# Kernel tuning notes

Measured on AMD Instinct MI355X. Metric: run time of the kernel, lower is better.

## Reference

```python
import jax, jax.numpy as jnp
import numpy as np

DIM = 512
T = 65536


def setup_inputs() -> dict:
    key = jax.random.key(0)
    k1, = jax.random.split(key, 1)
    z_rest = jax.random.normal(k1, (T, DIM), dtype=jnp.float32)
    # var_vbl = inv_softplus(sqrt(var_init)) with var_init=1.0 -> log(expm1(1.0))
    var_vbl = jnp.full((DIM,), float(np.log(np.expm1(1.0))), dtype=jnp.float32)
    # corr_vbl = inv_sigmoid(0.1) = log(0.1) - log(0.9)
    corr_vbl = jnp.full((DIM,), float(np.log(0.1) - np.log(0.9)), dtype=jnp.float32)
    prior_mu = jnp.zeros((DIM,), dtype=jnp.float32)
    return {"z_rest": z_rest, "var_vbl": var_vbl, "corr_vbl": corr_vbl, "prior_mu": prior_mu}


def reference(z_rest, var_vbl, corr_vbl, prior_mu):
    # init_train_lkd with z_context=None, starting from fresh state (sample_size=0).
    prior_var = jnp.square(jax.nn.softplus(var_vbl))          # [D]
    prior_cov = jax.nn.sigmoid(corr_vbl) * prior_var          # [D]
    two_pi = 2.0 * jnp.pi

    def step(carry, xs):
        mu, var, lkd = carry
        z, t = xs  # z: [D], t: scalar step index (== sample_size - 1 after increment)
        lkd = lkd + jnp.sum(-0.5 * jnp.log(two_pi * var)
                            - jnp.square(z - mu) / (2.0 * var))
        dd = prior_cov / (prior_var + prior_cov * t)
        mu = (1.0 - dd) * mu + z * dd
        var = (1.0 - dd) * var + (prior_var - prior_cov) * dd
        return (mu, var, lkd), None

    ts = jnp.arange(z_rest.shape[0], dtype=z_rest.dtype)
    init = (prior_mu.astype(z_rest.dtype), prior_var, jnp.zeros((), z_rest.dtype))
    (_, _, lkd), _ = jax.lax.scan(step, init, (z_rest, ts))
    return lkd
```

## Files before the change

### kernel.cpp

```cpp
#include <hip/hip_runtime.h>
#include <math.h>


#define DIM    512
#define TT     65536
#define CHUNKS 1024
#define ROWS   64
#define GROUPS 64
#define CPG    16

#define TWO_PI 6.283185307179586

__global__ __launch_bounds__(128) void k1_fused(const float* __restrict__ z,
                                                const float* __restrict__ var_vbl,
                                                const float* __restrict__ corr_vbl,
                                                const float* __restrict__ prior_mu,
                                                float* __restrict__ sums,
                                                float* __restrict__ s0a,
                                                float* __restrict__ s1a,
                                                float* __restrict__ s2a) {
    const int chunk = blockIdx.x;
    const int tid = threadIdx.x;
    const int d0 = tid * 4;
    const float t0m1 = (float)(chunk * ROWS) - 1.0f;

    float vv[4], cc[4], k0[4], L[4], S0[4], S1[4], S2[4], Dprev[4], invDprev[4];
#pragma unroll
    for (int j = 0; j < 4; ++j) {
        const int d = d0 + j;
        float spv = log1pf(expf(var_vbl[d]));
        float v = spv * spv;
        float c = v / (1.0f + expf(-corr_vbl[d]));
        vv[j] = v;
        cc[j] = c;
        k0[j] = (v - c) * prior_mu[d];
        L[j] = 0.f; S0[j] = 0.f; S1[j] = 0.f; S2[j] = 0.f;
        Dprev[j] = fmaf(c, t0m1, v);
        invDprev[j] = __builtin_amdgcn_rcpf(Dprev[j]);
    }

    const float4* zp = reinterpret_cast<const float4*>(z)
                       + (size_t)chunk * ROWS * (DIM / 4) + tid;
    float tf = t0m1 + 1.0f;
#pragma unroll 4
    for (int r = 0; r < ROWS; ++r) {
        float4 zv = zp[(size_t)r * (DIM / 4)];
        float zz[4] = {zv.x, zv.y, zv.z, zv.w};
#pragma unroll
        for (int j = 0; j < 4; ++j) {
            float Dt = fmaf(cc[j], tf, vv[j]);
            float invDt = __builtin_amdgcn_rcpf(Dt);
            float w = fmaf(Dprev[j], zz[j], -fmaf(cc[j], L[j], k0[j]));
            float rr = invDt * invDprev[j];
            S0[j] += rr;
            float rw = rr * w;
            S1[j] += rw;
            S2[j] = fmaf(rw, w, S2[j]);
            L[j] += zz[j];
            Dprev[j] = Dt;
            invDprev[j] = invDt;
        }
        tf += 1.0f;
    }

    const size_t o4 = (size_t)chunk * (DIM / 4) + tid;
    reinterpret_cast<float4*>(sums)[o4] = make_float4(L[0], L[1], L[2], L[3]);
    reinterpret_cast<float4*>(s0a)[o4] = make_float4(S0[0], S0[1], S0[2], S0[3]);
    reinterpret_cast<float4*>(s1a)[o4] = make_float4(S1[0], S1[1], S1[2], S1[3]);
    reinterpret_cast<float4*>(s2a)[o4] = make_float4(S2[0], S2[1], S2[2], S2[3]);
}

__global__ __launch_bounds__(512) void k2a_gsum(const float* __restrict__ sums,
                                                float* __restrict__ gsums) {
    const int g = blockIdx.x;
    const int d = threadIdx.x;
    float vals[CPG];
#pragma unroll
    for (int i = 0; i < CPG; ++i)
        vals[i] = sums[(size_t)(g * CPG + i) * DIM + d];
    float run = 0.f;
#pragma unroll
    for (int i = 0; i < CPG; ++i) run += vals[i];
    gsums[(size_t)g * DIM + d] = run;
}

__global__ __launch_bounds__(512) void k2b_scan(float* __restrict__ gsums,
                                                const float* __restrict__ var_vbl,
                                                const float* __restrict__ corr_vbl,
                                                float* __restrict__ out) {
    const int d = threadIdx.x;
    float vals[GROUPS];
#pragma unroll
    for (int g = 0; g < GROUPS; ++g)
        vals[g] = gsums[(size_t)g * DIM + d];
    float run = 0.f;
#pragma unroll
    for (int g = 0; g < GROUPS; ++g) {
        gsums[(size_t)g * DIM + d] = run;
        run += vals[g];
    }
    double sp = log1p(exp((double)var_vbl[d]));
    double v = sp * sp;
    double cc = v / (1.0 + exp(-(double)corr_vbl[d]));
    double vmc = v - cc;
    double Dlast = v + cc * (double)(TT - 1);
    double Ld = -0.5 * ((double)TT * (log(TWO_PI) + log(vmc)) + log(Dlast / vmc));
    __shared__ double red[512];
    red[d] = Ld;
    __syncthreads();
    for (int s = 256; s > 0; s >>= 1) {
        if (d < s) red[d] += red[d + s];
        __syncthreads();
    }
    if (d == 0) out[0] = (float)red[0];
}

__global__ __launch_bounds__(512) void k2c_combine(const float* __restrict__ sums,
                                                   const float* __restrict__ gsums,
                                                   const float* __restrict__ s0a,
                                                   const float* __restrict__ s1a,
                                                   const float* __restrict__ s2a,
                                                   const float* __restrict__ var_vbl,
                                                   const float* __restrict__ corr_vbl,
                                                   float* __restrict__ out) {
    const int g = blockIdx.x;
    const int d = threadIdx.x;
    float spv = log1pf(expf(var_vbl[d]));
    float v = spv * spv;
    float c = v / (1.0f + expf(-corr_vbl[d]));
    float kq = 0.5f / (v - c);

    float run = gsums[(size_t)g * DIM + d];
    float q = 0.f;
#pragma unroll
    for (int i = 0; i < CPG; ++i) {
        const size_t idx = (size_t)(g * CPG + i) * DIM + d;
        float s = sums[idx];
        float S0 = s0a[idx];
        float S1 = s1a[idx];
        float S2 = s2a[idx];
        float cP = c * run;
        q += kq * (S2 - 2.f * cP * S1 + cP * cP * S0);
        run += s;
    }

    for (int off = 32; off > 0; off >>= 1) q += __shfl_down(q, off, 64);
    __shared__ float wsred[8];
    const int lane = d & 63, w = d >> 6;
    if (lane == 0) wsred[w] = q;
    __syncthreads();
    if (d == 0) {
        float tot = 0.f;
#pragma unroll
        for (int i = 0; i < 8; ++i) tot += wsred[i];
        atomicAdd(out, -tot);
    }
}

extern "C" void kernel_launch(void* const* d_in, const int* in_sizes, int n_in,
                              void* d_out, int out_size, void* d_ws, size_t ws_size,
                              hipStream_t stream) {
    const float* z = (const float*)d_in[0];
    const float* var_vbl = (const float*)d_in[1];
    const float* corr_vbl = (const float*)d_in[2];
    const float* prior_mu = (const float*)d_in[3];
    float* out = (float*)d_out;
    float* sums = (float*)d_ws;
    float* s0a = sums + (size_t)CHUNKS * DIM;
    float* s1a = s0a + (size_t)CHUNKS * DIM;
    float* s2a = s1a + (size_t)CHUNKS * DIM;
    float* gsums = s2a + (size_t)CHUNKS * DIM;

    k1_fused<<<CHUNKS, 128, 0, stream>>>(z, var_vbl, corr_vbl, prior_mu,
                                         sums, s0a, s1a, s2a);
    k2a_gsum<<<GROUPS, 512, 0, stream>>>(sums, gsums);
    k2b_scan<<<1, 512, 0, stream>>>(gsums, var_vbl, corr_vbl, out);
    k2c_combine<<<GROUPS, 512, 0, stream>>>(sums, gsums, s0a, s1a, s2a,
                                            var_vbl, corr_vbl, out);
}
```

Baseline: 207.2 us.

## Fuse group-sum and scan kernels into combine via redundant prefix sums

Removes the separate group-sum and exclusive-scan kernels. Each combine block now recomputes its prefix by summing all preceding chunk sums directly, and block 0 adds the constant log-determinant term through an atomic. A memset zeroes the output up front. This drops two kernel launches and their serialization, at the cost of redundant, uneven prefix reads across blocks.

```diff
diff --git a/kernel.cpp b/kernel.cpp
--- a/kernel.cpp
+++ b/kernel.cpp
@@ -70,59 +70,13 @@
     reinterpret_cast<float4*>(s2a)[o4] = make_float4(S2[0], S2[1], S2[2], S2[3]);
 }
 
-__global__ __launch_bounds__(512) void k2a_gsum(const float* __restrict__ sums,
-                                                float* __restrict__ gsums) {
-    const int g = blockIdx.x;
-    const int d = threadIdx.x;
-    float vals[CPG];
-#pragma unroll
-    for (int i = 0; i < CPG; ++i)
-        vals[i] = sums[(size_t)(g * CPG + i) * DIM + d];
-    float run = 0.f;
-#pragma unroll
-    for (int i = 0; i < CPG; ++i) run += vals[i];
-    gsums[(size_t)g * DIM + d] = run;
-}
-
-__global__ __launch_bounds__(512) void k2b_scan(float* __restrict__ gsums,
-                                                const float* __restrict__ var_vbl,
-                                                const float* __restrict__ corr_vbl,
-                                                float* __restrict__ out) {
-    const int d = threadIdx.x;
-    float vals[GROUPS];
-#pragma unroll
-    for (int g = 0; g < GROUPS; ++g)
-        vals[g] = gsums[(size_t)g * DIM + d];
-    float run = 0.f;
-#pragma unroll
-    for (int g = 0; g < GROUPS; ++g) {
-        gsums[(size_t)g * DIM + d] = run;
-        run += vals[g];
-    }
-    double sp = log1p(exp((double)var_vbl[d]));
-    double v = sp * sp;
-    double cc = v / (1.0 + exp(-(double)corr_vbl[d]));
-    double vmc = v - cc;
-    double Dlast = v + cc * (double)(TT - 1);
-    double Ld = -0.5 * ((double)TT * (log(TWO_PI) + log(vmc)) + log(Dlast / vmc));
-    __shared__ double red[512];
-    red[d] = Ld;
-    __syncthreads();
-    for (int s = 256; s > 0; s >>= 1) {
-        if (d < s) red[d] += red[d + s];
-        __syncthreads();
-    }
-    if (d == 0) out[0] = (float)red[0];
-}
-
-__global__ __launch_bounds__(512) void k2c_combine(const float* __restrict__ sums,
-                                                   const float* __restrict__ gsums,
-                                                   const float* __restrict__ s0a,
-                                                   const float* __restrict__ s1a,
-                                                   const float* __restrict__ s2a,
-                                                   const float* __restrict__ var_vbl,
-                                                   const float* __restrict__ corr_vbl,
-                                                   float* __restrict__ out) {
+__global__ __launch_bounds__(512) void k2_combine(const float* __restrict__ sums,
+                                                  const float* __restrict__ s0a,
+                                                  const float* __restrict__ s1a,
+                                                  const float* __restrict__ s2a,
+                                                  const float* __restrict__ var_vbl,
+                                                  const float* __restrict__ corr_vbl,
+                                                  float* __restrict__ out) {
     const int g = blockIdx.x;
     const int d = threadIdx.x;
     float spv = log1pf(expf(var_vbl[d]));
@@ -130,7 +84,12 @@
     float c = v / (1.0f + expf(-corr_vbl[d]));
     float kq = 0.5f / (v - c);
 
-    float run = gsums[(size_t)g * DIM + d];
+    float run = 0.f;
+    const int nrows = g * CPG;
+#pragma unroll 8
+    for (int i = 0; i < nrows; ++i)
+        run += sums[(size_t)i * DIM + d];
+
     float q = 0.f;
 #pragma unroll
     for (int i = 0; i < CPG; ++i) {
@@ -155,6 +114,23 @@
         for (int i = 0; i < 8; ++i) tot += wsred[i];
         atomicAdd(out, -tot);
     }
+
+    if (g == 0) {
+        double sp = log1p(exp((double)var_vbl[d]));
+        double vd = sp * sp;
+        double cd = vd / (1.0 + exp(-(double)corr_vbl[d]));
+        double vmc = vd - cd;
+        double Dlast = vd + cd * (double)(TT - 1);
+        double Ld = -0.5 * ((double)TT * (log(TWO_PI) + log(vmc)) + log(Dlast / vmc));
+        __shared__ double redd[512];
+        redd[d] = Ld;
+        __syncthreads();
+        for (int s = 256; s > 0; s >>= 1) {
+            if (d < s) redd[d] += redd[d + s];
+            __syncthreads();
+        }
+        if (d == 0) atomicAdd(out, (float)redd[0]);
+    }
 }
 
 extern "C" void kernel_launch(void* const* d_in, const int* in_sizes, int n_in,
@@ -169,12 +145,10 @@
     float* s0a = sums + (size_t)CHUNKS * DIM;
     float* s1a = s0a + (size_t)CHUNKS * DIM;
     float* s2a = s1a + (size_t)CHUNKS * DIM;
-    float* gsums = s2a + (size_t)CHUNKS * DIM;
 
+    hipMemsetAsync(d_out, 0, sizeof(float), stream);
     k1_fused<<<CHUNKS, 128, 0, stream>>>(z, var_vbl, corr_vbl, prior_mu,
                                          sums, s0a, s1a, s2a);
-    k2a_gsum<<<GROUPS, 512, 0, stream>>>(sums, gsums);
-    k2b_scan<<<1, 512, 0, stream>>>(gsums, var_vbl, corr_vbl, out);
-    k2c_combine<<<GROUPS, 512, 0, stream>>>(sums, gsums, s0a, s1a, s2a,
-                                            var_vbl, corr_vbl, out);
+    k2_combine<<<GROUPS, 512, 0, stream>>>(sums, s0a, s1a, s2a,
+                                           var_vbl, corr_vbl, out);
 }
```

New measurement: 246.6 us. 1.19x slower.
